# Performance work log

Measured on AMD Instinct MI355X. Metric: run time of the kernel, lower is better.

The kernel has to match this reference:

```python
import jax, jax.numpy as jnp
import numpy as np

NUM_EMBEDDINGS = 1024
EMBEDDING_DIM = 64
COMMITMENT_COST = 0.25


def setup_inputs() -> dict:
    key = jax.random.key(0)
    k1, k2 = jax.random.split(key)
    z = jax.random.normal(k1, (32, EMBEDDING_DIM, 32, 32), dtype=jnp.float32)
    # matches nn.Embedding init: uniform(-1/K, 1/K)
    codebook = jax.random.uniform(
        k2, (NUM_EMBEDDINGS, EMBEDDING_DIM), dtype=jnp.float32,
        minval=-1.0 / NUM_EMBEDDINGS, maxval=1.0 / NUM_EMBEDDINGS)
    return {"z": z, "codebook": codebook}


def reference(z, codebook):
    B, C, H, W = z.shape  # C == embedding_dim
    zp = jnp.transpose(z, (0, 2, 3, 1))          # [B,H,W,C]
    z_flat = zp.reshape(-1, C)                    # [N,C], N=B*H*W
    # squared euclidean distances to every code: [N,K]
    d = (jnp.sum(z_flat ** 2, axis=1, keepdims=True)
         + jnp.sum(codebook ** 2, axis=1)
         - 2.0 * jnp.matmul(z_flat, codebook.T))
    indices = jnp.argmin(d, axis=1)               # [N]
    z_q = codebook[indices].reshape(zp.shape)     # [B,H,W,C]
    e_latent_loss = jnp.mean((jax.lax.stop_gradient(z_q) - zp) ** 2)
    q_latent_loss = jnp.mean((z_q - jax.lax.stop_gradient(zp)) ** 2)
    loss = q_latent_loss + COMMITMENT_COST * e_latent_loss
    # straight-through estimator
    z_q_st = zp + jax.lax.stop_gradient(z_q - zp)
    z_q_out = jnp.transpose(z_q_st, (0, 3, 1, 2))  # back to NCHW
    return z_q_out, loss, indices
```

## Files before the change

kernel.cpp:

```cpp
#include <hip/hip_runtime.h>
#include <float.h>


#define DIM       64
#define N_EMB     1024
#define N_PX      32768
#define LOSS_OFF  2097152
#define IDX_OFF   2097153
#define LOSS_SCALE 5.9604644775390625e-07f

__device__ __forceinline__ float np_sumsq64_row(const float* __restrict__ row) {
    #pragma clang fp contract(off)
    float r[8];
    #pragma unroll
    for (int j = 0; j < 8; ++j) {
        float s = row[j] * row[j];
        #pragma unroll
        for (int m = 1; m < 8; ++m) {
            float p = row[j + 8 * m] * row[j + 8 * m];
            s = s + p;
        }
        r[j] = s;
    }
    return ((r[0] + r[1]) + (r[2] + r[3])) + ((r[4] + r[5]) + (r[6] + r[7]));
}

__global__ __launch_bounds__(256, 4)
void vq_argmin(const float* __restrict__ z, const float* __restrict__ cb,
               float* __restrict__ ws_val, int* __restrict__ ws_idx,
               float* __restrict__ out) {
    __shared__ float4 ldsZ[16 * 64];
    __shared__ float  esq[256];
    __shared__ float  cand_val[4 * 64];
    __shared__ int    cand_idx[4 * 64];

    const int tid  = threadIdx.x;
    const int lane = tid & 63;
    const int wave = __builtin_amdgcn_readfirstlane(tid >> 6);
    const int g    = blockIdx.x >> 2;
    const int s    = blockIdx.x & 3;
    const int n0   = g * 64;
    const int b    = n0 >> 10;
    const int hw0  = n0 & 1023;
    const size_t zbase = (size_t)b * 65536 + (size_t)hw0;

    {
        const int px = tid & 63;
        const int cq = tid >> 6;
        #pragma unroll
        for (int r = 0; r < 4; ++r) {
            const int c4 = cq * 4 + r;
            const float* zp = z + zbase + (size_t)(c4 * 4) * 1024 + px;
            float4 v;
            v.x = zp[0];
            v.y = zp[1024];
            v.z = zp[2048];
            v.w = zp[3072];
            ldsZ[c4 * 64 + px] = v;
        }
    }

    esq[tid] = np_sumsq64_row(cb + (size_t)(s * 256 + tid) * DIM);

    __syncthreads();

    float zz;
    {
        #pragma clang fp contract(off)
        float4 qa = ldsZ[lane];
        float4 qb = ldsZ[64 + lane];
        float r0 = qa.x * qa.x, r1 = qa.y * qa.y, r2 = qa.z * qa.z, r3 = qa.w * qa.w;
        float r4 = qb.x * qb.x, r5 = qb.y * qb.y, r6 = qb.z * qb.z, r7 = qb.w * qb.w;
        #pragma unroll
        for (int m = 1; m < 8; ++m) {
            qa = ldsZ[(2 * m) * 64 + lane];
            qb = ldsZ[(2 * m + 1) * 64 + lane];
            float p;
            p = qa.x * qa.x; r0 = r0 + p;
            p = qa.y * qa.y; r1 = r1 + p;
            p = qa.z * qa.z; r2 = r2 + p;
            p = qa.w * qa.w; r3 = r3 + p;
            p = qb.x * qb.x; r4 = r4 + p;
            p = qb.y * qb.y; r5 = r5 + p;
            p = qb.z * qb.z; r6 = r6 + p;
            p = qb.w * qb.w; r7 = r7 + p;
        }
        zz = ((r0 + r1) + (r2 + r3)) + ((r4 + r5) + (r6 + r7));
    }

    float best = FLT_MAX;
    int   bidx = 0;
    const int kb = s * 256 + wave * 64;
    const int lb = wave * 64;
    for (int kk = 0; kk < 64; kk += 8) {
        const float* e = cb + (size_t)(kb + kk) * DIM;
        float d0 = 0.f, d1 = 0.f, d2 = 0.f, d3 = 0.f;
        float d4 = 0.f, d5 = 0.f, d6 = 0.f, d7 = 0.f;
        #pragma unroll
        for (int c4 = 0; c4 < 16; ++c4) {
            const float4 vzc = ldsZ[c4 * 64 + lane];
            const int c0 = c4 * 4;
#define VQ_FMA4(DJ, J) \
            DJ = __builtin_fmaf(e[(J)*DIM + c0    ], vzc.x, DJ); \
            DJ = __builtin_fmaf(e[(J)*DIM + c0 + 1], vzc.y, DJ); \
            DJ = __builtin_fmaf(e[(J)*DIM + c0 + 2], vzc.z, DJ); \
            DJ = __builtin_fmaf(e[(J)*DIM + c0 + 3], vzc.w, DJ);
            VQ_FMA4(d0, 0) VQ_FMA4(d1, 1) VQ_FMA4(d2, 2) VQ_FMA4(d3, 3)
            VQ_FMA4(d4, 4) VQ_FMA4(d5, 5) VQ_FMA4(d6, 6) VQ_FMA4(d7, 7)
#undef VQ_FMA4
        }
#define VQ_SCORE(DJ, J) \
        { \
            float sc; \
            { \
                _Pragma("clang fp contract(off)") \
                const float p = zz + esq[lb + kk + (J)]; \
                sc = p - 2.0f * DJ; \
            } \
            if (sc < best) { best = sc; bidx = kb + kk + (J); } \
        }
        VQ_SCORE(d0, 0) VQ_SCORE(d1, 1) VQ_SCORE(d2, 2) VQ_SCORE(d3, 3)
        VQ_SCORE(d4, 4) VQ_SCORE(d5, 5) VQ_SCORE(d6, 6) VQ_SCORE(d7, 7)
#undef VQ_SCORE
    }
    cand_val[wave * 64 + lane] = best;
    cand_idx[wave * 64 + lane] = bidx;
    __syncthreads();

    if (tid < 64) {
        float bv = cand_val[tid];
        int   bi = cand_idx[tid];
        #pragma unroll
        for (int w = 1; w < 4; ++w) {
            float v = cand_val[w * 64 + tid];
            int   i = cand_idx[w * 64 + tid];
            if (v < bv || (v == bv && i < bi)) { bv = v; bi = i; }
        }
        ws_val[s * N_PX + n0 + tid] = bv;
        ws_idx[s * N_PX + n0 + tid] = bi;
    }
    if (blockIdx.x == 0 && tid == 0) out[LOSS_OFF] = 0.f;
}

__global__ __launch_bounds__(256, 4)
void vq_out(const float* __restrict__ z, const float* __restrict__ cb,
            const float* __restrict__ ws_val, const int* __restrict__ ws_idx,
            float* __restrict__ out) {
    __shared__ int   fidx[64];
    __shared__ float lred[4];

    const int tid  = threadIdx.x;
    const int lane = tid & 63;
    const int wave = tid >> 6;
    const int n0   = blockIdx.x * 64;
    const int b    = n0 >> 10;
    const int hw0  = n0 & 1023;
    const size_t zbase = (size_t)b * 65536 + (size_t)hw0;

    if (tid < 64) {
        float bv = ws_val[n0 + tid];
        int   bi = ws_idx[n0 + tid];
        #pragma unroll
        for (int sl = 1; sl < 4; ++sl) {
            float v = ws_val[sl * N_PX + n0 + tid];
            int   i = ws_idx[sl * N_PX + n0 + tid];
            if (v < bv || (v == bv && i < bi)) { bv = v; bi = i; }
        }
        fidx[tid] = bi;
        out[IDX_OFF + n0 + tid] = (float)bi;
    }
    __syncthreads();

    const int px = tid & 63;
    const int cg = tid >> 6;
    const int mi = fidx[px];
    float lacc = 0.f;
    #pragma unroll
    for (int i = 0; i < 16; ++i) {
        const int c = cg * 16 + i;
        float q  = cb[mi * DIM + c];
        size_t go = zbase + (size_t)c * 1024 + px;
        float zv = z[go];
        float d  = q - zv;
        lacc = __builtin_fmaf(d, d, lacc);
        out[go] = q;
    }
    #pragma unroll
    for (int off = 32; off > 0; off >>= 1)
        lacc += __shfl_down(lacc, off, 64);
    if (lane == 0) lred[wave] = lacc;
    __syncthreads();
    if (tid == 0) {
        float t = (lred[0] + lred[1]) + (lred[2] + lred[3]);
        atomicAdd(&out[LOSS_OFF], t * LOSS_SCALE);
    }
}

extern "C" void kernel_launch(void* const* d_in, const int* in_sizes, int n_in,
                              void* d_out, int out_size, void* d_ws, size_t ws_size,
                              hipStream_t stream) {
    const float* z  = (const float*)d_in[0];
    const float* cb = (const float*)d_in[1];
    float* out = (float*)d_out;
    float* ws_val = (float*)d_ws;
    int*   ws_idx = (int*)((char*)d_ws + 4u * N_PX * sizeof(float));

    vq_argmin<<<2048, 256, 0, stream>>>(z, cb, ws_val, ws_idx, out);
    vq_out<<<512, 256, 0, stream>>>(z, cb, ws_val, ws_idx, out);
}
```

Before: 152.2 us.

## Stage codebook slice in LDS and compute two pixels per thread

Result: faster. 144.5 us (-5.1%).

```diff
diff --git a/kernel.cpp b/kernel.cpp
--- a/kernel.cpp
+++ b/kernel.cpp
@@ -25,115 +25,138 @@
     return ((r[0] + r[1]) + (r[2] + r[3])) + ((r[4] + r[5]) + (r[6] + r[7]));
 }
 
-__global__ __launch_bounds__(256, 4)
+__device__ __forceinline__ float np_sumsq64_lds(const float4* ldsZ, int px) {
+    #pragma clang fp contract(off)
+    float4 qa = ldsZ[px];
+    float4 qb = ldsZ[128 + px];
+    float r0 = qa.x * qa.x, r1 = qa.y * qa.y, r2 = qa.z * qa.z, r3 = qa.w * qa.w;
+    float r4 = qb.x * qb.x, r5 = qb.y * qb.y, r6 = qb.z * qb.z, r7 = qb.w * qb.w;
+    #pragma unroll
+    for (int m = 1; m < 8; ++m) {
+        qa = ldsZ[(2 * m) * 128 + px];
+        qb = ldsZ[(2 * m + 1) * 128 + px];
+        float p;
+        p = qa.x * qa.x; r0 = r0 + p;
+        p = qa.y * qa.y; r1 = r1 + p;
+        p = qa.z * qa.z; r2 = r2 + p;
+        p = qa.w * qa.w; r3 = r3 + p;
+        p = qb.x * qb.x; r4 = r4 + p;
+        p = qb.y * qb.y; r5 = r5 + p;
+        p = qb.z * qb.z; r6 = r6 + p;
+        p = qb.w * qb.w; r7 = r7 + p;
+    }
+    return ((r0 + r1) + (r2 + r3)) + ((r4 + r5) + (r6 + r7));
+}
+
+__global__ __launch_bounds__(256, 2)
 void vq_argmin(const float* __restrict__ z, const float* __restrict__ cb,
                float* __restrict__ ws_val, int* __restrict__ ws_idx,
                float* __restrict__ out) {
-    __shared__ float4 ldsZ[16 * 64];
-    __shared__ float  esq[256];
-    __shared__ float  cand_val[4 * 64];
-    __shared__ int    cand_idx[4 * 64];
+    __shared__ float4 ldsZ[16 * 128];
+    __shared__ float4 ldsE[128 * 16];
+    __shared__ float  esq[128];
+    __shared__ float  cand_val[4 * 128];
+    __shared__ int    cand_idx[4 * 128];
 
     const int tid  = threadIdx.x;
     const int lane = tid & 63;
     const int wave = __builtin_amdgcn_readfirstlane(tid >> 6);
-    const int g    = blockIdx.x >> 2;
-    const int s    = blockIdx.x & 3;
-    const int n0   = g * 64;
+    const int g    = blockIdx.x >> 3;
+    const int s    = blockIdx.x & 7;
+    const int n0   = g * 128;
     const int b    = n0 >> 10;
     const int hw0  = n0 & 1023;
     const size_t zbase = (size_t)b * 65536 + (size_t)hw0;
 
     {
-        const int px = tid & 63;
-        const int cq = tid >> 6;
-        #pragma unroll
-        for (int r = 0; r < 4; ++r) {
-            const int c4 = cq * 4 + r;
+        const int px = tid & 127;
+        const int cq = tid >> 7;
+        #pragma unroll
+        for (int r = 0; r < 8; ++r) {
+            const int c4 = cq * 8 + r;
             const float* zp = z + zbase + (size_t)(c4 * 4) * 1024 + px;
             float4 v;
             v.x = zp[0];
             v.y = zp[1024];
             v.z = zp[2048];
             v.w = zp[3072];
-            ldsZ[c4 * 64 + px] = v;
-        }
-    }
-
-    esq[tid] = np_sumsq64_row(cb + (size_t)(s * 256 + tid) * DIM);
-
-    __syncthreads();
-
-    float zz;
+            ldsZ[c4 * 128 + px] = v;
+        }
+    }
     {
-        #pragma clang fp contract(off)
-        float4 qa = ldsZ[lane];
-        float4 qb = ldsZ[64 + lane];
-        float r0 = qa.x * qa.x, r1 = qa.y * qa.y, r2 = qa.z * qa.z, r3 = qa.w * qa.w;
-        float r4 = qb.x * qb.x, r5 = qb.y * qb.y, r6 = qb.z * qb.z, r7 = qb.w * qb.w;
-        #pragma unroll
-        for (int m = 1; m < 8; ++m) {
-            qa = ldsZ[(2 * m) * 64 + lane];
-            qb = ldsZ[(2 * m + 1) * 64 + lane];
-            float p;
-            p = qa.x * qa.x; r0 = r0 + p;
-            p = qa.y * qa.y; r1 = r1 + p;
-            p = qa.z * qa.z; r2 = r2 + p;
-            p = qa.w * qa.w; r3 = r3 + p;
-            p = qb.x * qb.x; r4 = r4 + p;
-            p = qb.y * qb.y; r5 = r5 + p;
-            p = qb.z * qb.z; r6 = r6 + p;
-            p = qb.w * qb.w; r7 = r7 + p;
-        }
-        zz = ((r0 + r1) + (r2 + r3)) + ((r4 + r5) + (r6 + r7));
-    }
-
-    float best = FLT_MAX;
-    int   bidx = 0;
-    const int kb = s * 256 + wave * 64;
-    const int lb = wave * 64;
-    for (int kk = 0; kk < 64; kk += 8) {
-        const float* e = cb + (size_t)(kb + kk) * DIM;
-        float d0 = 0.f, d1 = 0.f, d2 = 0.f, d3 = 0.f;
-        float d4 = 0.f, d5 = 0.f, d6 = 0.f, d7 = 0.f;
+        const float4* cb4 = (const float4*)(cb + (size_t)s * 128 * DIM);
+        #pragma unroll
+        for (int r = 0; r < 8; ++r)
+            ldsE[r * 256 + tid] = cb4[r * 256 + tid];
+    }
+    if (tid < 128)
+        esq[tid] = np_sumsq64_row(cb + (size_t)(s * 128 + tid) * DIM);
+
+    __syncthreads();
+
+    const float zz0 = np_sumsq64_lds(ldsZ, lane);
+    const float zz1 = np_sumsq64_lds(ldsZ, lane + 64);
+
+    float best0 = FLT_MAX, best1 = FLT_MAX;
+    int   bidx0 = 0,       bidx1 = 0;
+    const int kb = s * 128 + wave * 32;
+    const int lw = wave * 32;
+    for (int kk = 0; kk < 32; kk += 8) {
+        float d00 = 0.f, d01 = 0.f, d02 = 0.f, d03 = 0.f;
+        float d04 = 0.f, d05 = 0.f, d06 = 0.f, d07 = 0.f;
+        float d10 = 0.f, d11 = 0.f, d12 = 0.f, d13 = 0.f;
+        float d14 = 0.f, d15 = 0.f, d16 = 0.f, d17 = 0.f;
         #pragma unroll
         for (int c4 = 0; c4 < 16; ++c4) {
-            const float4 vzc = ldsZ[c4 * 64 + lane];
-            const int c0 = c4 * 4;
-#define VQ_FMA4(DJ, J) \
-            DJ = __builtin_fmaf(e[(J)*DIM + c0    ], vzc.x, DJ); \
-            DJ = __builtin_fmaf(e[(J)*DIM + c0 + 1], vzc.y, DJ); \
-            DJ = __builtin_fmaf(e[(J)*DIM + c0 + 2], vzc.z, DJ); \
-            DJ = __builtin_fmaf(e[(J)*DIM + c0 + 3], vzc.w, DJ);
-            VQ_FMA4(d0, 0) VQ_FMA4(d1, 1) VQ_FMA4(d2, 2) VQ_FMA4(d3, 3)
-            VQ_FMA4(d4, 4) VQ_FMA4(d5, 5) VQ_FMA4(d6, 6) VQ_FMA4(d7, 7)
-#undef VQ_FMA4
-        }
-#define VQ_SCORE(DJ, J) \
+            const float4 z0 = ldsZ[c4 * 128 + lane];
+            const float4 z1 = ldsZ[c4 * 128 + 64 + lane];
+#define VQ_CODE(J) \
+            { \
+                const float4 e4 = ldsE[(lw + kk + (J)) * 16 + c4];  \
+                d0##J = __builtin_fmaf(e4.x, z0.x, d0##J); \
+                d0##J = __builtin_fmaf(e4.y, z0.y, d0##J); \
+                d0##J = __builtin_fmaf(e4.z, z0.z, d0##J); \
+                d0##J = __builtin_fmaf(e4.w, z0.w, d0##J); \
+                d1##J = __builtin_fmaf(e4.x, z1.x, d1##J); \
+                d1##J = __builtin_fmaf(e4.y, z1.y, d1##J); \
+                d1##J = __builtin_fmaf(e4.z, z1.z, d1##J); \
+                d1##J = __builtin_fmaf(e4.w, z1.w, d1##J); \
+            }
+            VQ_CODE(0) VQ_CODE(1) VQ_CODE(2) VQ_CODE(3)
+            VQ_CODE(4) VQ_CODE(5) VQ_CODE(6) VQ_CODE(7)
+#undef VQ_CODE
+        }
+#define VQ_SCORE(J) \
         { \
-            float sc; \
+            const float ee = esq[lw + kk + (J)]; \
+            float sc0, sc1; \
             { \
                 _Pragma("clang fp contract(off)") \
-                const float p = zz + esq[lb + kk + (J)]; \
-                sc = p - 2.0f * DJ; \
+                const float p0 = zz0 + ee; \
+                const float p1 = zz1 + ee; \
+                sc0 = p0 - 2.0f * d0##J; \
+                sc1 = p1 - 2.0f * d1##J; \
             } \
-            if (sc < best) { best = sc; bidx = kb + kk + (J); } \
-        }
-        VQ_SCORE(d0, 0) VQ_SCORE(d1, 1) VQ_SCORE(d2, 2) VQ_SCORE(d3, 3)
-        VQ_SCORE(d4, 4) VQ_SCORE(d5, 5) VQ_SCORE(d6, 6) VQ_SCORE(d7, 7)
+            if (sc0 < best0) { best0 = sc0; bidx0 = kb + kk + (J); } \
+            if (sc1 < best1) { best1 = sc1; bidx1 = kb + kk + (J); } \
+        }
+        VQ_SCORE(0) VQ_SCORE(1) VQ_SCORE(2) VQ_SCORE(3)
+        VQ_SCORE(4) VQ_SCORE(5) VQ_SCORE(6) VQ_SCORE(7)
 #undef VQ_SCORE
     }
-    cand_val[wave * 64 + lane] = best;
-    cand_idx[wave * 64 + lane] = bidx;
-    __syncthreads();
-
-    if (tid < 64) {
+    cand_val[wave * 128 + lane]      = best0;
+    cand_idx[wave * 128 + lane]      = bidx0;
+    cand_val[wave * 128 + 64 + lane] = best1;
+    cand_idx[wave * 128 + 64 + lane] = bidx1;
+    __syncthreads();
+
+    if (tid < 128) {
         float bv = cand_val[tid];
         int   bi = cand_idx[tid];
         #pragma unroll
         for (int w = 1; w < 4; ++w) {
-            float v = cand_val[w * 64 + tid];
-            int   i = cand_idx[w * 64 + tid];
+            float v = cand_val[w * 128 + tid];
+            int   i = cand_idx[w * 128 + tid];
             if (v < bv || (v == bv && i < bi)) { bv = v; bi = i; }
         }
         ws_val[s * N_PX + n0 + tid] = bv;
@@ -161,7 +184,7 @@
         float bv = ws_val[n0 + tid];
         int   bi = ws_idx[n0 + tid];
         #pragma unroll
-        for (int sl = 1; sl < 4; ++sl) {
+        for (int sl = 1; sl < 8; ++sl) {
             float v = ws_val[sl * N_PX + n0 + tid];
             int   i = ws_idx[sl * N_PX + n0 + tid];
             if (v < bv || (v == bv && i < bi)) { bv = v; bi = i; }
@@ -203,7 +226,7 @@
     const float* cb = (const float*)d_in[1];
     float* out = (float*)d_out;
     float* ws_val = (float*)d_ws;
-    int*   ws_idx = (int*)((char*)d_ws + 4u * N_PX * sizeof(float));
+    int*   ws_idx = (int*)((char*)d_ws + 8u * N_PX * sizeof(float));
 
     vq_argmin<<<2048, 256, 0, stream>>>(z, cb, ws_val, ws_idx, out);
     vq_out<<<512, 256, 0, stream>>>(z, cb, ws_val, ws_idx, out);
```
